# Performance work log

Hardware: AMD Instinct MI355X
Metric: run time of the kernel (lower is better)

The kernel has to match this reference:

```python
import jax, jax.numpy as jnp
import numpy as np

B, N, D = 4, 2048, 1024
H = 16
HD = D // H  # head_dim = 64
SCALE = HD ** -0.5


def setup_inputs() -> dict:
    key = jax.random.key(0)
    k1, k2, k3, k4 = jax.random.split(key, 4)
    x = jax.random.normal(k1, (B, N, D), dtype=jnp.float32)
    # init-scale weights for numerically sane softmax logits
    w_qkv = jax.random.normal(k2, (3 * D, D), dtype=jnp.float32) * 0.02
    w_proj = jax.random.normal(k3, (D, D), dtype=jnp.float32) * 0.02
    b_proj = jax.random.normal(k4, (D,), dtype=jnp.float32) * 0.02
    return {"x": x, "w_qkv": w_qkv, "w_proj": w_proj, "b_proj": b_proj}


def reference(x, w_qkv, w_proj, b_proj):
    # qkv projection (width_mult=1.0 -> Dyna slicing is identity; qkv_bias=False)
    qkv = jnp.einsum('bnd,ed->bne', x, w_qkv)          # (B, N, 3D)
    qkv = qkv.reshape(B, N, 3, H, HD)
    q = qkv[:, :, 0].transpose(0, 2, 1, 3)              # (B, H, N, HD)
    k = qkv[:, :, 1].transpose(0, 2, 1, 3)
    v = qkv[:, :, 2].transpose(0, 2, 1, 3)
    q = q * SCALE
    attn = jnp.einsum('bhqd,bhkd->bhqk', q, k)          # (B, H, N, N)
    attn = jax.nn.softmax(attn, axis=-1)
    out = jnp.einsum('bhqk,bhkd->bhqd', attn, v)        # (B, H, N, HD)
    out = out.transpose(0, 2, 1, 3).reshape(B, N, D)
    # output projection (bias=True)
    return jnp.einsum('bnd,ed->bne', out, w_proj) + b_proj
```

## Files before the change

kernel.cpp:

```cpp
#include <hip/hip_runtime.h>
#include <hip/hip_bf16.h>
#include <stdint.h>


typedef __attribute__((ext_vector_type(8))) short short8;
typedef __attribute__((ext_vector_type(4))) short short4v;
typedef __attribute__((ext_vector_type(4))) float float4v;

#define MFMA16(a, b, c) __builtin_amdgcn_mfma_f32_16x16x32_bf16((a), (b), (c), 0, 0, 0)
#define MFMA16K16(a, b, c) __builtin_amdgcn_mfma_f32_16x16x16bf16_1k((a), (b), (c), 0, 0, 0)

static __device__ __forceinline__ unsigned short f2bf(float f) {
  union { float f; unsigned u; } v; v.f = f;
  unsigned r = v.u + 0x7fffu + ((v.u >> 16) & 1u);
  return (unsigned short)(r >> 16);
}
static __device__ __forceinline__ float bf2f(unsigned short u) {
  union { unsigned u; float f; } v; v.u = ((unsigned)u) << 16;
  return v.f;
}
static __device__ __forceinline__ unsigned pkbf(float a, float b) {
  union { __hip_bfloat162 v; unsigned u; } c;
  c.v = __float22bfloat162_rn(make_float2(a, b));
  return c.u;
}
static __device__ __forceinline__ float4v fzero() {
  float4v z; z[0] = 0.f; z[1] = 0.f; z[2] = 0.f; z[3] = 0.f; return z;
}
static __device__ __forceinline__ void load_lds16(const void* g, void* l) {
  typedef const __attribute__((address_space(1))) void* gp_t;
  typedef __attribute__((address_space(3))) void* lp_t;
  __builtin_amdgcn_global_load_lds((gp_t)(uintptr_t)g, (lp_t)(uint32_t)(uintptr_t)l, 16, 0, 0);
}

__global__ void detect_dtype(const unsigned short* __restrict__ x, int* flag) {
  __shared__ int cnt;
  if (threadIdx.x == 0) cnt = 0;
  __syncthreads();
  int c = 0;
  for (int i = threadIdx.x; i < 4096; i += 256) {
    const unsigned v = x[i] & 0x7FFFu;
    if ((v >> 7) >= 134u) ++c;
  }
  atomicAdd(&cnt, c);
  __syncthreads();
  if (threadIdx.x == 0) *flag = (cnt > 64) ? 1 : 0;
}

static __device__ __forceinline__ void cv8(const void* src, unsigned short* dst,
                                           int i, int fl) {
  if (fl) {
    const float* s = (const float*)src + i;
    short8 o;
    for (int j = 0; j < 8; ++j) o[j] = (short)f2bf(s[j]);
    *(short8*)(dst + i) = o;
  } else {
    *(short8*)(dst + i) = *(const short8*)((const unsigned short*)src + i);
  }
}
__global__ __launch_bounds__(256) void convert_all(
    const void* __restrict__ s0, const void* __restrict__ s1,
    const void* __restrict__ s2, const void* __restrict__ s3,
    unsigned short* __restrict__ d0, unsigned short* __restrict__ d1,
    unsigned short* __restrict__ d2, unsigned short* __restrict__ d3,
    const int* __restrict__ flag) {
  const int t = blockIdx.x * 256 + threadIdx.x;
  const int fl = *flag;
  if (t < 1048576)       cv8(s0, d0, t * 8, fl);
  else if (t < 1441792)  cv8(s1, d1, (t - 1048576) * 8, fl);
  else if (t < 1572864)  cv8(s2, d2, (t - 1441792) * 8, fl);
  else if (t < 1572992)  cv8(s3, d3, (t - 1572864) * 8, fl);
}

__global__ __launch_bounds__(256) void qkv_gemm(
    const unsigned short* __restrict__ X, const unsigned short* __restrict__ W,
    unsigned short* __restrict__ Qo, unsigned short* __restrict__ Ko,
    unsigned short* __restrict__ Vt) {
  __shared__ __attribute__((aligned(16))) unsigned short lA[128 * 32];
  __shared__ __attribute__((aligned(16))) unsigned short lB[128 * 32];
  const int tid = threadIdx.x;
  const int wave = tid >> 6, lane = tid & 63, quad = lane >> 4, l16 = lane & 15;
  const int wm = wave >> 1, wn = wave & 1;
  const int m0 = blockIdx.x * 128, n0 = blockIdx.y * 128;

  float4v acc[4][4];
  for (int i = 0; i < 4; ++i) for (int j = 0; j < 4; ++j) acc[i][j] = fzero();

  const int f0 = tid, f1 = 256 + tid;
  const int r0 = f0 >> 2, c0 = (f0 & 3) * 8;
  const int r1 = f1 >> 2, c1 = (f1 & 3) * 8;
  unsigned short* dA0 = lA + (wave * 64) * 8;
  unsigned short* dA1 = lA + (256 + wave * 64) * 8;
  unsigned short* dB0 = lB + (wave * 64) * 8;
  unsigned short* dB1 = lB + (256 + wave * 64) * 8;

  for (int k0 = 0; k0 < 1024; k0 += 32) {
    __syncthreads();
    load_lds16(X + (size_t)(m0 + r0) * 1024 + k0 + c0, dA0);
    load_lds16(X + (size_t)(m0 + r1) * 1024 + k0 + c1, dA1);
    load_lds16(W + (size_t)(n0 + r0) * 1024 + k0 + c0, dB0);
    load_lds16(W + (size_t)(n0 + r1) * 1024 + k0 + c1, dB1);
    __syncthreads();
    short8 af[4], bfr[4];
    for (int t = 0; t < 4; ++t) {
      af[t]  = *(const short8*)(lA + (wm * 64 + t * 16 + l16) * 32 + quad * 8);
      bfr[t] = *(const short8*)(lB + (wn * 64 + t * 16 + l16) * 32 + quad * 8);
    }
    for (int mt = 0; mt < 4; ++mt)
      for (int nt = 0; nt < 4; ++nt)
        acc[mt][nt] = MFMA16(af[mt], bfr[nt], acc[mt][nt]);
  }

  for (int mt = 0; mt < 4; ++mt) {
    const int mbase = m0 + wm * 64 + mt * 16 + quad * 4;
    const int b = mbase >> 11;
    const int nrow = mbase & 2047;
    for (int nt = 0; nt < 4; ++nt) {
      const int e = n0 + wn * 64 + nt * 16 + l16;
      const int c = e >> 10, h = (e >> 6) & 15, hd = e & 63;
      const int bh = b * 16 + h;
      if (c == 0) {
        for (int r = 0; r < 4; ++r)
          Qo[((size_t)bh * 2048 + nrow + r) * 64 + hd] = f2bf(acc[mt][nt][r] * 0.125f);
      } else if (c == 1) {
        for (int r = 0; r < 4; ++r)
          Ko[((size_t)bh * 2048 + nrow + r) * 64 + hd] = f2bf(acc[mt][nt][r]);
      } else {
        short4v pk;
        for (int r = 0; r < 4; ++r) pk[r] = (short)f2bf(acc[mt][nt][r]);
        *(short4v*)(Vt + ((size_t)bh * 64 + hd) * 2048 + nrow) = pk;
      }
    }
  }
}

__global__ __launch_bounds__(256, 4) void flash_attn(
    const unsigned short* __restrict__ Q, const unsigned short* __restrict__ K,
    const unsigned short* __restrict__ Vt, unsigned short* __restrict__ AO) {
  __shared__ __attribute__((aligned(16))) unsigned short lK[64 * 72];
  __shared__ __attribute__((aligned(16))) unsigned short lV[64 * 72];
  const int tid = threadIdx.x;
  const int wave = tid >> 6, lane = tid & 63, quad = lane >> 4, l16 = lane & 15;
  const int qt = blockIdx.x, bh = blockIdx.y;
  const int b = bh >> 4, h = bh & 15;
  const size_t base = (size_t)bh * 2048 * 64;
  const unsigned short* Qp = Q + base;
  const unsigned short* Kp = K + base;
  const unsigned short* Vp = Vt + base;
  const int q0 = qt * 128;

  const int qa = q0 + wave * 16 + l16;
  const short8 qfA0 = *(const short8*)(Qp + (size_t)qa * 64 + quad * 8);
  const short8 qfA1 = *(const short8*)(Qp + (size_t)qa * 64 + 32 + quad * 8);
  const short8 qfB0 = *(const short8*)(Qp + (size_t)(qa + 64) * 64 + quad * 8);
  const short8 qfB1 = *(const short8*)(Qp + (size_t)(qa + 64) * 64 + 32 + quad * 8);

  float4v oaccA[4], oaccB[4];
  for (int i = 0; i < 4; ++i) { oaccA[i] = fzero(); oaccB[i] = fzero(); }
  float lsumA = 0.f, lsumB = 0.f;

  const int f0 = tid, f1 = 256 + tid;
  const int sk0 = (f0 >> 3) * 72 + (f0 & 7) * 8;
  const int sk1 = (f1 >> 3) * 72 + (f1 & 7) * 8;

  for (int kb = 0; kb < 32; ++kb) {
    const short8 kv0 = *(const short8*)(Kp + (size_t)kb * 4096 + f0 * 8);
    const short8 kv1 = *(const short8*)(Kp + (size_t)kb * 4096 + f1 * 8);
    const short8 vv0 = *(const short8*)(Vp + (size_t)(f0 >> 3) * 2048 + kb * 64 + (f0 & 7) * 8);
    const short8 vv1 = *(const short8*)(Vp + (size_t)(f1 >> 3) * 2048 + kb * 64 + (f1 & 7) * 8);
    __syncthreads();
    *(short8*)(lK + sk0) = kv0;
    *(short8*)(lK + sk1) = kv1;
    *(short8*)(lV + sk0) = vv0;
    *(short8*)(lV + sk1) = vv1;
    __syncthreads();

    float4v sA[4], sB[4];
    for (int t = 0; t < 4; ++t) {
      const short8 k0f = *(const short8*)(lK + (t * 16 + l16) * 72 + quad * 8);
      const short8 k1f = *(const short8*)(lK + (t * 16 + l16) * 72 + 32 + quad * 8);
      sA[t] = MFMA16(k0f, qfA0, fzero());
      sA[t] = MFMA16(k1f, qfA1, sA[t]);
      sB[t] = MFMA16(k0f, qfB0, fzero());
      sB[t] = MFMA16(k1f, qfB1, sB[t]);
    }

    short4v pA[4], pB[4];
    for (int t = 0; t < 4; ++t) {
      float eA0 = __expf(sA[t][0]), eA1 = __expf(sA[t][1]);
      float eA2 = __expf(sA[t][2]), eA3 = __expf(sA[t][3]);
      float eB0 = __expf(sB[t][0]), eB1 = __expf(sB[t][1]);
      float eB2 = __expf(sB[t][2]), eB3 = __expf(sB[t][3]);
      lsumA += (eA0 + eA1) + (eA2 + eA3);
      lsumB += (eB0 + eB1) + (eB2 + eB3);
      union { unsigned u[2]; short4v s; } ca, cb;
      ca.u[0] = pkbf(eA0, eA1); ca.u[1] = pkbf(eA2, eA3);
      cb.u[0] = pkbf(eB0, eB1); cb.u[1] = pkbf(eB2, eB3);
      pA[t] = ca.s; pB[t] = cb.s;
    }

    for (int nt = 0; nt < 4; ++nt) {
      const unsigned short* vrow = lV + (nt * 16 + l16) * 72 + quad * 4;
      for (int t = 0; t < 4; ++t) {
        const short4v vf = *(const short4v*)(vrow + t * 16);
        oaccA[nt] = MFMA16K16(vf, pA[t], oaccA[nt]);
        oaccB[nt] = MFMA16K16(vf, pB[t], oaccB[nt]);
      }
    }
  }

  lsumA += __shfl_xor(lsumA, 16); lsumA += __shfl_xor(lsumA, 32);
  lsumB += __shfl_xor(lsumB, 16); lsumB += __shfl_xor(lsumB, 32);
  const float invA = 1.f / lsumA, invB = 1.f / lsumB;

  unsigned short* aoA = AO + ((size_t)(b * 2048 + qa)) * 1024 + h * 64 + quad * 4;
  unsigned short* aoB = aoA + (size_t)64 * 1024;
  for (int nt = 0; nt < 4; ++nt) {
    union { unsigned u[2]; short4v s; } oa, ob;
    oa.u[0] = pkbf(oaccA[nt][0] * invA, oaccA[nt][1] * invA);
    oa.u[1] = pkbf(oaccA[nt][2] * invA, oaccA[nt][3] * invA);
    ob.u[0] = pkbf(oaccB[nt][0] * invB, oaccB[nt][1] * invB);
    ob.u[1] = pkbf(oaccB[nt][2] * invB, oaccB[nt][3] * invB);
    *(short4v*)(aoA + nt * 16) = oa.s;
    *(short4v*)(aoB + nt * 16) = ob.s;
  }
}

__global__ __launch_bounds__(256) void proj_gemm(
    const unsigned short* __restrict__ A, const unsigned short* __restrict__ W,
    const unsigned short* __restrict__ bias_bf, const void* __restrict__ bias_raw,
    void* __restrict__ outv, const int* __restrict__ flag) {
  __shared__ __attribute__((aligned(16))) unsigned short lA[128 * 32];
  __shared__ __attribute__((aligned(16))) unsigned short lB[128 * 32];
  const int tid = threadIdx.x;
  const int wave = tid >> 6, lane = tid & 63, quad = lane >> 4, l16 = lane & 15;
  const int wm = wave >> 1, wn = wave & 1;
  const int m0 = blockIdx.x * 128, n0 = blockIdx.y * 128;
  const int fl = *flag;

  float4v acc[4][4];
  for (int i = 0; i < 4; ++i) for (int j = 0; j < 4; ++j) acc[i][j] = fzero();

  const int f0 = tid, f1 = 256 + tid;
  const int r0 = f0 >> 2, c0 = (f0 & 3) * 8;
  const int r1 = f1 >> 2, c1 = (f1 & 3) * 8;
  unsigned short* dA0 = lA + (wave * 64) * 8;
  unsigned short* dA1 = lA + (256 + wave * 64) * 8;
  unsigned short* dB0 = lB + (wave * 64) * 8;
  unsigned short* dB1 = lB + (256 + wave * 64) * 8;

  for (int k0 = 0; k0 < 1024; k0 += 32) {
    __syncthreads();
    load_lds16(A + (size_t)(m0 + r0) * 1024 + k0 + c0, dA0);
    load_lds16(A + (size_t)(m0 + r1) * 1024 + k0 + c1, dA1);
    load_lds16(W + (size_t)(n0 + r0) * 1024 + k0 + c0, dB0);
    load_lds16(W + (size_t)(n0 + r1) * 1024 + k0 + c1, dB1);
    __syncthreads();
    short8 af[4], bfr[4];
    for (int t = 0; t < 4; ++t) {
      af[t]  = *(const short8*)(lA + (wm * 64 + t * 16 + l16) * 32 + quad * 8);
      bfr[t] = *(const short8*)(lB + (wn * 64 + t * 16 + l16) * 32 + quad * 8);
    }
    for (int mt = 0; mt < 4; ++mt)
      for (int nt = 0; nt < 4; ++nt)
        acc[mt][nt] = MFMA16(af[mt], bfr[nt], acc[mt][nt]);
  }

  for (int mt = 0; mt < 4; ++mt) {
    const int mbase = m0 + wm * 64 + mt * 16 + quad * 4;
    for (int nt = 0; nt < 4; ++nt) {
      const int e = n0 + wn * 64 + nt * 16 + l16;
      const float bv = fl ? ((const float*)bias_raw)[e] : bf2f(bias_bf[e]);
      for (int r = 0; r < 4; ++r) {
        const float val = acc[mt][nt][r] + bv;
        const size_t idx = (size_t)(mbase + r) * 1024 + e;
        if (fl) ((float*)outv)[idx] = val;
        else    ((unsigned short*)outv)[idx] = f2bf(val);
      }
    }
  }
}

extern "C" void kernel_launch(void* const* d_in, const int* in_sizes, int n_in,
                              void* d_out, int out_size, void* d_ws, size_t ws_size,
                              hipStream_t stream) {
  const void* x_raw     = d_in[0];
  const void* wqkv_raw  = d_in[1];
  const void* wproj_raw = d_in[2];
  const void* bproj_raw = d_in[3];

  const size_t NE = (size_t)4 * 16 * 2048 * 64;
  unsigned short* ws = (unsigned short*)d_ws;
  unsigned short* Q      = ws;
  unsigned short* K      = Q + NE;
  unsigned short* Vt     = K + NE;
  unsigned short* xb     = Vt + NE;
  unsigned short* AO     = xb;
  unsigned short* wqkvb  = xb + NE;
  unsigned short* wprojb = wqkvb + 3145728;
  unsigned short* bprojb = wprojb + 1048576;
  int* flag = (int*)(bprojb + 1024);

  detect_dtype<<<1, 256, 0, stream>>>((const unsigned short*)x_raw, flag);
  convert_all<<<6145, 256, 0, stream>>>(x_raw, wqkv_raw, wproj_raw, bproj_raw,
                                        xb, wqkvb, wprojb, bprojb, flag);

  qkv_gemm<<<dim3(64, 24), 256, 0, stream>>>(xb, wqkvb, Q, K, Vt);
  flash_attn<<<dim3(16, 64), 256, 0, stream>>>(Q, K, Vt, AO);
  proj_gemm<<<dim3(64, 8), 256, 0, stream>>>(AO, wprojb, bprojb, bproj_raw,
                                             d_out, flag);
}
```

Baseline: 291.2 us.

## Double-buffer K/V tiles, swizzle V layout, and use native exp2 with log2e-folded scale

The flash attention kernel gets double-buffered shared-memory K/V tiles. The next tile is prefetched into registers during compute and stored to the other buffer afterwards, which removes one barrier per iteration and hides global load latency. The V tile is stored with an interleaved layout so each lane fetches its four k-slices with two 16-byte LDS reads instead of four 8-byte reads. The softmax exp is replaced by native exp2, with log2(e) folded into the Q scaling in the QKV projection, which trades a little precision for cheaper transcendental evaluation.

```diff
diff --git a/kernel.cpp b/kernel.cpp
--- a/kernel.cpp
+++ b/kernel.cpp
@@ -9,6 +9,8 @@
 
 #define MFMA16(a, b, c) __builtin_amdgcn_mfma_f32_16x16x32_bf16((a), (b), (c), 0, 0, 0)
 #define MFMA16K16(a, b, c) __builtin_amdgcn_mfma_f32_16x16x16bf16_1k((a), (b), (c), 0, 0, 0)
+
+extern "C" __device__ float __ocml_native_exp2_f32(float);
 
 static __device__ __forceinline__ unsigned short f2bf(float f) {
   union { float f; unsigned u; } v; v.f = f;
@@ -121,7 +123,8 @@
       const int bh = b * 16 + h;
       if (c == 0) {
         for (int r = 0; r < 4; ++r)
-          Qo[((size_t)bh * 2048 + nrow + r) * 64 + hd] = f2bf(acc[mt][nt][r] * 0.125f);
+          Qo[((size_t)bh * 2048 + nrow + r) * 64 + hd] =
+              f2bf(acc[mt][nt][r] * 0.18033688011112042f);
       } else if (c == 1) {
         for (int r = 0; r < 4; ++r)
           Ko[((size_t)bh * 2048 + nrow + r) * 64 + hd] = f2bf(acc[mt][nt][r]);
@@ -137,8 +140,8 @@
 __global__ __launch_bounds__(256, 4) void flash_attn(
     const unsigned short* __restrict__ Q, const unsigned short* __restrict__ K,
     const unsigned short* __restrict__ Vt, unsigned short* __restrict__ AO) {
-  __shared__ __attribute__((aligned(16))) unsigned short lK[64 * 72];
-  __shared__ __attribute__((aligned(16))) unsigned short lV[64 * 72];
+  __shared__ __attribute__((aligned(16))) unsigned short lK[2][64 * 72];
+  __shared__ __attribute__((aligned(16))) unsigned short lV[2][64 * 72];
   const int tid = threadIdx.x;
   const int wave = tid >> 6, lane = tid & 63, quad = lane >> 4, l16 = lane & 15;
   const int qt = blockIdx.x, bh = blockIdx.y;
@@ -160,25 +163,47 @@
   float lsumA = 0.f, lsumB = 0.f;
 
   const int f0 = tid, f1 = 256 + tid;
-  const int sk0 = (f0 >> 3) * 72 + (f0 & 7) * 8;
-  const int sk1 = (f1 >> 3) * 72 + (f1 & 7) * 8;
+  const int skK0 = (f0 >> 3) * 72 + (f0 & 7) * 8;
+  const int skK1 = (f1 >> 3) * 72 + (f1 & 7) * 8;
+  const int jv0 = f0 & 7, jv1 = f1 & 7;
+  const int svL0 = (f0 >> 3) * 72 + ((2 * jv0) & 3) * 16 + (jv0 >> 1) * 4;
+  const int svH0 = (f0 >> 3) * 72 + ((2 * jv0 + 1) & 3) * 16 + (jv0 >> 1) * 4;
+  const int svL1 = (f1 >> 3) * 72 + ((2 * jv1) & 3) * 16 + (jv1 >> 1) * 4;
+  const int svH1 = (f1 >> 3) * 72 + ((2 * jv1 + 1) & 3) * 16 + (jv1 >> 1) * 4;
+
+  union s8u { short8 v8; short4v v4[2]; };
+
+  s8u kv0, kv1, vv0, vv1;
+  kv0.v8 = *(const short8*)(Kp + (size_t)f0 * 8);
+  kv1.v8 = *(const short8*)(Kp + (size_t)f1 * 8);
+  vv0.v8 = *(const short8*)(Vp + (size_t)(f0 >> 3) * 2048 + jv0 * 8);
+  vv1.v8 = *(const short8*)(Vp + (size_t)(f1 >> 3) * 2048 + jv1 * 8);
+  *(short8*)(lK[0] + skK0) = kv0.v8;
+  *(short8*)(lK[0] + skK1) = kv1.v8;
+  *(short4v*)(lV[0] + svL0) = vv0.v4[0];
+  *(short4v*)(lV[0] + svH0) = vv0.v4[1];
+  *(short4v*)(lV[0] + svL1) = vv1.v4[0];
+  *(short4v*)(lV[0] + svH1) = vv1.v4[1];
 
   for (int kb = 0; kb < 32; ++kb) {
-    const short8 kv0 = *(const short8*)(Kp + (size_t)kb * 4096 + f0 * 8);
-    const short8 kv1 = *(const short8*)(Kp + (size_t)kb * 4096 + f1 * 8);
-    const short8 vv0 = *(const short8*)(Vp + (size_t)(f0 >> 3) * 2048 + kb * 64 + (f0 & 7) * 8);
-    const short8 vv1 = *(const short8*)(Vp + (size_t)(f1 >> 3) * 2048 + kb * 64 + (f1 & 7) * 8);
-    __syncthreads();
-    *(short8*)(lK + sk0) = kv0;
-    *(short8*)(lK + sk1) = kv1;
-    *(short8*)(lV + sk0) = vv0;
-    *(short8*)(lV + sk1) = vv1;
-    __syncthreads();
+    const int cur = kb & 1;
+    if (kb < 31) {
+      const size_t ko = (size_t)(kb + 1) * 4096;
+      const int vo = (kb + 1) * 64;
+      kv0.v8 = *(const short8*)(Kp + ko + f0 * 8);
+      kv1.v8 = *(const short8*)(Kp + ko + f1 * 8);
+      vv0.v8 = *(const short8*)(Vp + (size_t)(f0 >> 3) * 2048 + vo + jv0 * 8);
+      vv1.v8 = *(const short8*)(Vp + (size_t)(f1 >> 3) * 2048 + vo + jv1 * 8);
+    }
+    __syncthreads();
+
+    const unsigned short* lKc = lK[cur];
+    const unsigned short* lVc = lV[cur];
 
     float4v sA[4], sB[4];
     for (int t = 0; t < 4; ++t) {
-      const short8 k0f = *(const short8*)(lK + (t * 16 + l16) * 72 + quad * 8);
-      const short8 k1f = *(const short8*)(lK + (t * 16 + l16) * 72 + 32 + quad * 8);
+      const short8 k0f = *(const short8*)(lKc + (t * 16 + l16) * 72 + quad * 8);
+      const short8 k1f = *(const short8*)(lKc + (t * 16 + l16) * 72 + 32 + quad * 8);
       sA[t] = MFMA16(k0f, qfA0, fzero());
       sA[t] = MFMA16(k1f, qfA1, sA[t]);
       sB[t] = MFMA16(k0f, qfB0, fzero());
@@ -187,10 +212,14 @@
 
     short4v pA[4], pB[4];
     for (int t = 0; t < 4; ++t) {
-      float eA0 = __expf(sA[t][0]), eA1 = __expf(sA[t][1]);
-      float eA2 = __expf(sA[t][2]), eA3 = __expf(sA[t][3]);
-      float eB0 = __expf(sB[t][0]), eB1 = __expf(sB[t][1]);
-      float eB2 = __expf(sB[t][2]), eB3 = __expf(sB[t][3]);
+      float eA0 = __ocml_native_exp2_f32(sA[t][0]);
+      float eA1 = __ocml_native_exp2_f32(sA[t][1]);
+      float eA2 = __ocml_native_exp2_f32(sA[t][2]);
+      float eA3 = __ocml_native_exp2_f32(sA[t][3]);
+      float eB0 = __ocml_native_exp2_f32(sB[t][0]);
+      float eB1 = __ocml_native_exp2_f32(sB[t][1]);
+      float eB2 = __ocml_native_exp2_f32(sB[t][2]);
+      float eB3 = __ocml_native_exp2_f32(sB[t][3]);
       lsumA += (eA0 + eA1) + (eA2 + eA3);
       lsumB += (eB0 + eB1) + (eB2 + eB3);
       union { unsigned u[2]; short4v s; } ca, cb;
@@ -200,12 +229,28 @@
     }
 
     for (int nt = 0; nt < 4; ++nt) {
-      const unsigned short* vrow = lV + (nt * 16 + l16) * 72 + quad * 4;
-      for (int t = 0; t < 4; ++t) {
-        const short4v vf = *(const short4v*)(vrow + t * 16);
-        oaccA[nt] = MFMA16K16(vf, pA[t], oaccA[nt]);
-        oaccB[nt] = MFMA16K16(vf, pB[t], oaccB[nt]);
-      }
+      const unsigned short* vrow = lVc + (nt * 16 + l16) * 72 + quad * 16;
+      s8u v01, v23;
+      v01.v8 = *(const short8*)(vrow);
+      v23.v8 = *(const short8*)(vrow + 8);
+      oaccA[nt] = MFMA16K16(v01.v4[0], pA[0], oaccA[nt]);
+      oaccA[nt] = MFMA16K16(v01.v4[1], pA[1], oaccA[nt]);
+      oaccA[nt] = MFMA16K16(v23.v4[0], pA[2], oaccA[nt]);
+      oaccA[nt] = MFMA16K16(v23.v4[1], pA[3], oaccA[nt]);
+      oaccB[nt] = MFMA16K16(v01.v4[0], pB[0], oaccB[nt]);
+      oaccB[nt] = MFMA16K16(v01.v4[1], pB[1], oaccB[nt]);
+      oaccB[nt] = MFMA16K16(v23.v4[0], pB[2], oaccB[nt]);
+      oaccB[nt] = MFMA16K16(v23.v4[1], pB[3], oaccB[nt]);
+    }
+
+    if (kb < 31) {
+      const int nxt = 1 - cur;
+      *(short8*)(lK[nxt] + skK0) = kv0.v8;
+      *(short8*)(lK[nxt] + skK1) = kv1.v8;
+      *(short4v*)(lV[nxt] + svL0) = vv0.v4[0];
+      *(short4v*)(lV[nxt] + svH0) = vv0.v4[1];
+      *(short4v*)(lV[nxt] + svL1) = vv1.v4[0];
+      *(short4v*)(lV[nxt] + svH1) = vv1.v4[1];
     }
   }
 
```

After: 301.0 us. +3.4%, slower.
